# Performance work log

Measured on AMD Instinct MI355X. Metric: run time of the kernel, lower is better.

## Reference

```python
import jax, jax.numpy as jnp
import numpy as np

N, E, D, H, C, K = 100000, 1250000, 64, 64, 40, 2


def setup_inputs() -> dict:
    key = jax.random.key(0)
    ks = jax.random.split(key, 10)
    s_in = 1.0 / np.sqrt(D)
    s_cat = 1.0 / np.sqrt(H * (K + 1))
    return {
        "x": jax.random.normal(ks[0], (N, D), jnp.float32),
        "edge_index": jax.random.randint(ks[1], (2, E), 0, N, dtype=jnp.int64),
        "W_ego": jax.random.normal(ks[2], (D, H), jnp.float32) * s_in,
        "b_ego": jnp.zeros((H,), jnp.float32),
        "W_conv": jax.random.normal(ks[3], (K, D, H), jnp.float32) * s_in,
        "b_conv": jnp.zeros((K, H), jnp.float32),
        "W_cls": jax.random.normal(ks[4], (H * (K + 1), C), jnp.float32) * s_cat,
        "b_cls": jnp.zeros((C,), jnp.float32),
    }


def _gcn_norm(edge_index, n):
    # PyG GCNConv default: add self-loops, symmetric normalization.
    row = jnp.concatenate([edge_index[0], jnp.arange(n, dtype=edge_index.dtype)])
    col = jnp.concatenate([edge_index[1], jnp.arange(n, dtype=edge_index.dtype)])
    deg = jax.ops.segment_sum(jnp.ones_like(col, dtype=jnp.float32), col, num_segments=n)
    dis = jnp.where(deg > 0, jax.lax.rsqrt(jnp.maximum(deg, 1.0)), 0.0)
    norm = dis[row] * dis[col]  # [E+N]
    return row, col, norm


def _gcn_conv(h, W, b, row, col, norm, n):
    hw = h @ W                                   # [N, H] transform first (cheap d)
    msg = norm[:, None] * hw[row]                # gather + scale, [E+N, H]
    agg = jax.ops.segment_sum(msg, col, num_segments=n)  # scatter-add to targets
    return agg + b


def reference(x, edge_index, W_ego, b_ego, W_conv, b_conv, W_cls, b_cls):
    n = x.shape[0]
    row, col, norm = _gcn_norm(edge_index, n)
    parts = [jax.nn.relu(x @ W_ego + b_ego)]
    h = x
    for k in range(K):
        h = jax.nn.relu(_gcn_conv(h, W_conv[k], b_conv[k], row, col, norm, n))
        parts.append(h)
    out = jnp.concatenate(parts, axis=-1)        # [N, H*(K+1)]
    # dropout is identity at inference (training=False)
    return out @ W_cls + b_cls
```

## Files before the change

### kernel.cpp

```cpp
#include <hip/hip_runtime.h>

using u16 = unsigned short;
using u32 = unsigned int;
using u64 = unsigned long long;
using short8 = __attribute__((ext_vector_type(8))) short;
using f32x4  = __attribute__((ext_vector_type(4))) float;

static inline int cdiv(long long a, long long b) { return (int)((a + b - 1) / b); }

__device__ __forceinline__ u16 f2bf(float x) {
    u32 u = __builtin_bit_cast(u32, x);
    u += 0x7fffu + ((u >> 16) & 1u);
    return (u16)(u >> 16);
}
__device__ __forceinline__ float bf2f(u16 h) {
    u32 u = ((u32)h) << 16;
    return __builtin_bit_cast(float, u);
}

#define BKT_SH 10
#define CHUNK 4096

__global__ __launch_bounds__(256) void k_bhist(const int* __restrict__ ei,
                                               int* __restrict__ bcntg, int E) {
    __shared__ int lb[128];
    if (threadIdx.x < 128) lb[threadIdx.x] = 0;
    __syncthreads();
    const int eb = blockIdx.x * CHUNK;
#pragma unroll
    for (int k = 0; k < 16; ++k) {
        int e = eb + k * 256 + threadIdx.x;
        if (e < E) atomicAdd(&lb[ei[E + e] >> BKT_SH], 1);
    }
    __syncthreads();
    if (threadIdx.x < 128 && lb[threadIdx.x] > 0)
        atomicAdd(&bcntg[threadIdx.x], lb[threadIdx.x]);
}

__global__ __launch_bounds__(128) void k_bscan(const int* __restrict__ bcntg,
                                               int* __restrict__ bbase,
                                               int* __restrict__ bcursor, int NB) {
    __shared__ int s[128];
    int t = threadIdx.x;
    int v = (t < NB) ? bcntg[t] : 0;
    s[t] = v;
    __syncthreads();
    for (int st = 1; st < 128; st <<= 1) {
        int add = (t >= st) ? s[t - st] : 0;
        __syncthreads();
        s[t] += add;
        __syncthreads();
    }
    int excl = s[t] - v;
    if (t < NB) { bbase[t] = excl; bcursor[t] = excl; }
    if (t == NB - 1) bbase[NB] = excl + v;
}

__global__ __launch_bounds__(256) void k_passA(const int* __restrict__ ei,
                                               int* __restrict__ bcursor,
                                               u64* __restrict__ sta, int E) {
    __shared__ int lcnt[128];
    __shared__ int lcur[128];
    if (threadIdx.x < 128) lcnt[threadIdx.x] = 0;
    __syncthreads();
    const int eb = blockIdx.x * CHUNK;
    int er[16], ec[16];
#pragma unroll
    for (int k = 0; k < 16; ++k) {
        int e = eb + k * 256 + threadIdx.x;
        if (e < E) {
            er[k] = ei[e];
            ec[k] = ei[E + e];
            atomicAdd(&lcnt[ec[k] >> BKT_SH], 1);
        } else {
            ec[k] = -1;
        }
    }
    __syncthreads();
    if (threadIdx.x < 128)
        lcur[threadIdx.x] = lcnt[threadIdx.x] > 0
                          ? atomicAdd(&bcursor[threadIdx.x], lcnt[threadIdx.x]) : 0;
    __syncthreads();
#pragma unroll
    for (int k = 0; k < 16; ++k) {
        if (ec[k] >= 0) {
            int pos = atomicAdd(&lcur[ec[k] >> BKT_SH], 1);
            sta[pos] = ((u64)(u32)ec[k] << 32) | (u32)er[k];
        }
    }
}

__global__ __launch_bounds__(256) void k_passB(const u64* __restrict__ sta,
                                               const int* __restrict__ bbase,
                                               int* __restrict__ indptr,
                                               float* __restrict__ dis,
                                               int* __restrict__ rows,
                                               int N, int NB) {
    __shared__ int lcnt[1024];
    __shared__ int cur[1024];
    __shared__ int ps[256];
    const int b = blockIdx.x;
    const int t = threadIdx.x;
    const int base = b << BKT_SH;
    const int e0 = bbase[b], e1 = bbase[b + 1];

#pragma unroll
    for (int k = 0; k < 4; ++k) lcnt[k * 256 + t] = 0;
    __syncthreads();
    for (int e = e0 + t; e < e1; e += 256)
        atomicAdd(&lcnt[(int)(sta[e] >> 32) - base], 1);
    __syncthreads();

    int a0 = lcnt[t * 4 + 0], a1 = lcnt[t * 4 + 1];
    int a2 = lcnt[t * 4 + 2], a3 = lcnt[t * 4 + 3];
    int sum = a0 + a1 + a2 + a3;
    ps[t] = sum;
    __syncthreads();
    for (int st = 1; st < 256; st <<= 1) {
        int add = (t >= st) ? ps[t - st] : 0;
        __syncthreads();
        ps[t] += add;
        __syncthreads();
    }
    int ex = e0 + ps[t] - sum;
    int exs[4] = {ex, ex + a0, ex + a0 + a1, ex + a0 + a1 + a2};
    int cnts[4] = {a0, a1, a2, a3};
#pragma unroll
    for (int k = 0; k < 4; ++k) {
        int j = t * 4 + k;
        cur[j] = exs[k];
        int node = base + j;
        if (node < N) {
            indptr[node] = exs[k];
            dis[node] = rsqrtf((float)cnts[k] + 1.0f);
        }
    }
    if (b == NB - 1 && t == 0) indptr[N] = bbase[NB];
    __syncthreads();

    for (int e = e0 + t; e < e1; e += 256) {
        u64 v = sta[e];
        int c = (int)(v >> 32);
        int pos = atomicAdd(&cur[c - base], 1);
        rows[pos] = (int)(u32)v;
    }
}

__global__ __launch_bounds__(256) void k_cast(const float* __restrict__ x,
                                              u32* __restrict__ xb, long long n8) {
    long long t = (long long)blockIdx.x * 256 + threadIdx.x;
    if (t >= n8) return;
    const float4* xp = (const float4*)(x + t * 8);
    float4 v0 = xp[0], v1 = xp[1];
    u32* o = xb + t * 4;
    o[0] = (u32)f2bf(v0.x) | ((u32)f2bf(v0.y) << 16);
    o[1] = (u32)f2bf(v0.z) | ((u32)f2bf(v0.w) << 16);
    o[2] = (u32)f2bf(v1.x) | ((u32)f2bf(v1.y) << 16);
    o[3] = (u32)f2bf(v1.z) | ((u32)f2bf(v1.w) << 16);
}

__global__ __launch_bounds__(256) void k_prep(const float* __restrict__ Wego,
                                              const float* __restrict__ Wconv,
                                              const float* __restrict__ Wcls,
                                              u16* __restrict__ WTin,
                                              u16* __restrict__ WTc0,
                                              u16* __restrict__ WT1,
                                              u16* __restrict__ WT2) {
    int t = blockIdx.x * 256 + threadIdx.x;
    int seg = t >> 6;
    int d = t & 63;
    if (seg < 128) {
        float v = (seg < 64) ? Wconv[d * 64 + seg] : Wego[d * 64 + (seg - 64)];
        WTin[seg * 64 + d] = f2bf(v);
    } else if (seg < 176) {
        int c = seg - 128;
        WTc0[c * 64 + d] = f2bf(c < 40 ? Wcls[d * 40 + c] : 0.f);
    } else if (seg < 288) {
        int c = seg - 176;
        float v = 0.f;
        if (c < 64) v = Wconv[64 * 64 + d * 64 + c];
        else if (c < 104) v = Wcls[(64 + d) * 40 + (c - 64)];
        WT1[c * 64 + d] = f2bf(v);
    } else if (seg < 336) {
        int c = seg - 288;
        WT2[c * 64 + d] = f2bf(c < 40 ? Wcls[(128 + d) * 40 + c] : 0.f);
    }
}

__global__ __launch_bounds__(256) void k_in(const u16* __restrict__ xb,
                                            const u16* __restrict__ WTin,
                                            const float* __restrict__ dis,
                                            const float* __restrict__ bego,
                                            u16* __restrict__ hws1,
                                            u16* __restrict__ p0, int N) {
    const int wid = (blockIdx.x * 256 + threadIdx.x) >> 6;
    const int l = threadIdx.x & 63;
    if (wid * 16 >= N) return;
    const int lr = l & 15;
    const int lk = l >> 4;

    const u16* arow = xb + ((size_t)(wid * 16 + lr)) * 64 + lk * 8;
    short8 a0 = *(const short8*)arow;
    short8 a1 = *(const short8*)(arow + 32);

    float dvals[4];
#pragma unroll
    for (int rg = 0; rg < 4; ++rg) dvals[rg] = dis[wid * 16 + lk * 4 + rg];

    for (int ct = 0; ct < 8; ++ct) {
        const u16* wrow = WTin + ((size_t)(ct * 16 + lr)) * 64 + lk * 8;
        short8 b0 = *(const short8*)wrow;
        short8 b1 = *(const short8*)(wrow + 32);
        f32x4 acc = {0.f, 0.f, 0.f, 0.f};
        acc = __builtin_amdgcn_mfma_f32_16x16x32_bf16(a0, b0, acc, 0, 0, 0);
        acc = __builtin_amdgcn_mfma_f32_16x16x32_bf16(a1, b1, acc, 0, 0, 0);
        const int col = ct * 16 + lr;
        if (col < 64) {
#pragma unroll
            for (int rg = 0; rg < 4; ++rg) {
                int r = wid * 16 + lk * 4 + rg;
                hws1[(size_t)r * 64 + col] = f2bf(dvals[rg] * acc[rg]);
            }
        } else {
            float be = bego[col - 64];
#pragma unroll
            for (int rg = 0; rg < 4; ++rg) {
                int r = wid * 16 + lk * 4 + rg;
                p0[(size_t)r * 64 + (col - 64)] = f2bf(fmaxf(acc[rg] + be, 0.f));
            }
        }
    }
}

__global__ __launch_bounds__(256) void k_cls0(const u16* __restrict__ p0,
                                              const u16* __restrict__ WTc0,
                                              const float* __restrict__ bcls,
                                              float* __restrict__ out, int N) {
    const int wid = (blockIdx.x * 256 + threadIdx.x) >> 6;
    const int l = threadIdx.x & 63;
    if (wid * 16 >= N) return;
    const int lr = l & 15;
    const int lk = l >> 4;

    const u16* arow = p0 + ((size_t)(wid * 16 + lr)) * 64 + lk * 8;
    short8 a0 = *(const short8*)arow;
    short8 a1 = *(const short8*)(arow + 32);

    for (int ct = 0; ct < 3; ++ct) {
        const u16* wrow = WTc0 + ((size_t)(ct * 16 + lr)) * 64 + lk * 8;
        short8 b0 = *(const short8*)wrow;
        short8 b1 = *(const short8*)(wrow + 32);
        f32x4 acc = {0.f, 0.f, 0.f, 0.f};
        acc = __builtin_amdgcn_mfma_f32_16x16x32_bf16(a0, b0, acc, 0, 0, 0);
        acc = __builtin_amdgcn_mfma_f32_16x16x32_bf16(a1, b1, acc, 0, 0, 0);
        const int col = ct * 16 + lr;
        if (col < 40) {
            float bc = bcls[col];
#pragma unroll
            for (int rg = 0; rg < 4; ++rg) {
                int r = wid * 16 + lk * 4 + rg;
                out[(size_t)r * 40 + col] = bc + acc[rg];
            }
        }
    }
}

__global__ __launch_bounds__(512) void k_gather(const int* __restrict__ indptr,
                                                const int* __restrict__ rows,
                                                const float* __restrict__ dis,
                                                const float* __restrict__ bconv,
                                                const u16* __restrict__ hws_in,
                                                u16* __restrict__ h, int N) {
    const int w = threadIdx.x >> 6;
    const int f = threadIdx.x & 63;
    const int i = blockIdx.x * 8 + w;
    if (i >= N) return;

    float acc = bf2f(hws_in[(size_t)i * 64 + f]);
    int p0 = __builtin_amdgcn_readfirstlane(indptr[i]);
    int p1 = __builtin_amdgcn_readfirstlane(indptr[i + 1]);
    int p = p0;
    for (; p + 8 <= p1; p += 8) {
        int r0 = rows[p + 0], r1 = rows[p + 1], r2 = rows[p + 2], r3 = rows[p + 3];
        int r4 = rows[p + 4], r5 = rows[p + 5], r6 = rows[p + 6], r7 = rows[p + 7];
        u16 v0 = hws_in[(size_t)r0 * 64 + f];
        u16 v1 = hws_in[(size_t)r1 * 64 + f];
        u16 v2 = hws_in[(size_t)r2 * 64 + f];
        u16 v3 = hws_in[(size_t)r3 * 64 + f];
        u16 v4 = hws_in[(size_t)r4 * 64 + f];
        u16 v5 = hws_in[(size_t)r5 * 64 + f];
        u16 v6 = hws_in[(size_t)r6 * 64 + f];
        u16 v7 = hws_in[(size_t)r7 * 64 + f];
        acc += ((bf2f(v0) + bf2f(v1)) + (bf2f(v2) + bf2f(v3))) +
               ((bf2f(v4) + bf2f(v5)) + (bf2f(v6) + bf2f(v7)));
    }
    for (; p + 4 <= p1; p += 4) {
        int r0 = rows[p + 0], r1 = rows[p + 1], r2 = rows[p + 2], r3 = rows[p + 3];
        u16 v0 = hws_in[(size_t)r0 * 64 + f];
        u16 v1 = hws_in[(size_t)r1 * 64 + f];
        u16 v2 = hws_in[(size_t)r2 * 64 + f];
        u16 v3 = hws_in[(size_t)r3 * 64 + f];
        acc += (bf2f(v0) + bf2f(v1)) + (bf2f(v2) + bf2f(v3));
    }
    for (; p < p1; ++p) acc += bf2f(hws_in[(size_t)rows[p] * 64 + f]);

    float hv = fmaxf(fmaf(dis[i], acc, bconv[f]), 0.0f);
    h[(size_t)i * 64 + f] = f2bf(hv);
}

template <int NC, bool HAS_NEXT>
__global__ __launch_bounds__(256) void k_mlp(const u16* __restrict__ h,
                                             const u16* __restrict__ WT,
                                             const float* __restrict__ dis,
                                             u16* __restrict__ hws_out,
                                             float* __restrict__ out, int N) {
    const int wid = (blockIdx.x * 256 + threadIdx.x) >> 6;
    const int l = threadIdx.x & 63;
    if (wid * 16 >= N) return;
    const int lr = l & 15;
    const int lk = l >> 4;

    const u16* hrow = h + ((size_t)(wid * 16 + lr)) * 64 + lk * 8;
    short8 a0 = *(const short8*)hrow;
    short8 a1 = *(const short8*)(hrow + 32);

    float dvals[4];
    if (HAS_NEXT) {
#pragma unroll
        for (int rg = 0; rg < 4; ++rg) dvals[rg] = dis[wid * 16 + lk * 4 + rg];
    }

    for (int ct = 0; ct < NC; ++ct) {
        const u16* wrow = WT + ((size_t)(ct * 16 + lr)) * 64 + lk * 8;
        short8 b0 = *(const short8*)wrow;
        short8 b1 = *(const short8*)(wrow + 32);
        f32x4 acc = {0.f, 0.f, 0.f, 0.f};
        acc = __builtin_amdgcn_mfma_f32_16x16x32_bf16(a0, b0, acc, 0, 0, 0);
        acc = __builtin_amdgcn_mfma_f32_16x16x32_bf16(a1, b1, acc, 0, 0, 0);
        const int col = ct * 16 + lr;
#pragma unroll
        for (int rg = 0; rg < 4; ++rg) {
            const int r = wid * 16 + lk * 4 + rg;
            if (HAS_NEXT) {
                if (col < 64) {
                    hws_out[(size_t)r * 64 + col] = f2bf(dvals[rg] * acc[rg]);
                } else {
                    int oc = col - 64;
                    if (oc < 40) out[(size_t)r * 40 + oc] += acc[rg];
                }
            } else {
                if (col < 40) out[(size_t)r * 40 + col] += acc[rg];
            }
        }
    }
}

extern "C" void kernel_launch(void* const* d_in, const int* in_sizes, int n_in,
                              void* d_out, int out_size, void* d_ws, size_t ws_size,
                              hipStream_t stream) {
    const float* x     = (const float*)d_in[0];
    const int*   ei    = (const int*)d_in[1];
    const float* Wego  = (const float*)d_in[2];
    const float* bego  = (const float*)d_in[3];
    const float* Wconv = (const float*)d_in[4];
    const float* bconv = (const float*)d_in[5];
    const float* Wcls  = (const float*)d_in[6];
    const float* bcls  = (const float*)d_in[7];
    float* out = (float*)d_out;

    const int N = in_sizes[0] / 64;
    const int E = in_sizes[1] / 2;
    const int NB = cdiv(N, 1 << BKT_SH);

    u16* xb   = (u16*)d_ws;
    u64* sta  = (u64*)d_ws;
    u16* hws1 = xb + (size_t)N * 64;
    u16* hws2 = hws1 + (size_t)N * 64;
    u16* hp   = hws2 + (size_t)N * 64;
    u16* WTin = hp + (size_t)N * 64;
    u16* WTc0 = WTin + 128 * 64;
    u16* WT1  = WTc0 + 48 * 64;
    u16* WT2  = WT1 + 112 * 64;
    float* dis = (float*)(WT2 + 48 * 64);
    int* indptr  = (int*)(dis + N);
    int* bcntg   = indptr + N + 1024;
    int* bbase   = bcntg + 128;
    int* bcursor = bbase + 132;
    int* rows    = bcursor + 128;

    hipMemsetAsync(bcntg, 0, 128 * sizeof(int), stream);

    k_bhist<<<cdiv(E, CHUNK), 256, 0, stream>>>(ei, bcntg, E);
    k_bscan<<<1, 128, 0, stream>>>(bcntg, bbase, bcursor, NB);
    k_passA<<<cdiv(E, CHUNK), 256, 0, stream>>>(ei, bcursor, sta, E);
    k_passB<<<NB, 256, 0, stream>>>(sta, bbase, indptr, dis, rows, N, NB);

    k_cast<<<cdiv((long long)N * 8, 256), 256, 0, stream>>>(x, (u32*)xb, (long long)N * 8);
    k_prep<<<cdiv(336 * 64, 256), 256, 0, stream>>>(Wego, Wconv, Wcls, WTin, WTc0, WT1, WT2);
    k_in<<<cdiv(cdiv(N, 16), 4), 256, 0, stream>>>(xb, WTin, dis, bego, hws1, hp, N);
    k_cls0<<<cdiv(cdiv(N, 16), 4), 256, 0, stream>>>(hp, WTc0, bcls, out, N);

    const int n_rt = cdiv(N, 16);
    k_gather<<<cdiv(N, 8), 512, 0, stream>>>(indptr, rows, dis, bconv, hws1, hp, N);
    k_mlp<7, true><<<cdiv(n_rt, 4), 256, 0, stream>>>(hp, WT1, dis, hws2, out, N);
    k_gather<<<cdiv(N, 8), 512, 0, stream>>>(indptr, rows, dis, bconv + 64, hws2, hp, N);
    k_mlp<3, false><<<cdiv(n_rt, 4), 256, 0, stream>>>(hp, WT2, dis, nullptr, out, N);
}
```

Baseline: 223.3 us.

## Fuse classifier into one concatenated GEMM, pack sort keys to 32 bits, drop cast kernel

The sort keys shrink from 64-bit (col,row) pairs to 32-bit words holding the local column in the high bits and the row in the low 17 bits. This halves the sort-buffer traffic but assumes N < 2^17. The bf16 cast of x is folded into the input GEMM kernel, and the three partial classifier GEMMs, which did read-modify-write on the fp32 output, are replaced by one final GEMM over a concatenated [N,192] hidden buffer. The aim is fewer launches and less output traffic, at the cost of a wider strided hidden buffer.

```diff
diff --git a/kernel.cpp b/kernel.cpp
--- a/kernel.cpp
+++ b/kernel.cpp
@@ -2,7 +2,6 @@
 
 using u16 = unsigned short;
 using u32 = unsigned int;
-using u64 = unsigned long long;
 using short8 = __attribute__((ext_vector_type(8))) short;
 using f32x4  = __attribute__((ext_vector_type(4))) float;
 
@@ -19,6 +18,7 @@
 }
 
 #define BKT_SH 10
+#define BKT_MASK ((1 << BKT_SH) - 1)
 #define CHUNK 4096
 
 __global__ __launch_bounds__(256) void k_bhist(const int* __restrict__ ei,
@@ -58,7 +58,7 @@
 
 __global__ __launch_bounds__(256) void k_passA(const int* __restrict__ ei,
                                                int* __restrict__ bcursor,
-                                               u64* __restrict__ sta, int E) {
+                                               u32* __restrict__ sta, int E) {
     __shared__ int lcnt[128];
     __shared__ int lcur[128];
     if (threadIdx.x < 128) lcnt[threadIdx.x] = 0;
@@ -85,12 +85,12 @@
     for (int k = 0; k < 16; ++k) {
         if (ec[k] >= 0) {
             int pos = atomicAdd(&lcur[ec[k] >> BKT_SH], 1);
-            sta[pos] = ((u64)(u32)ec[k] << 32) | (u32)er[k];
-        }
-    }
-}
-
-__global__ __launch_bounds__(256) void k_passB(const u64* __restrict__ sta,
+            sta[pos] = ((u32)(ec[k] & BKT_MASK) << 17) | (u32)er[k];
+        }
+    }
+}
+
+__global__ __launch_bounds__(256) void k_passB(const u32* __restrict__ sta,
                                                const int* __restrict__ bbase,
                                                int* __restrict__ indptr,
                                                float* __restrict__ dis,
@@ -108,7 +108,7 @@
     for (int k = 0; k < 4; ++k) lcnt[k * 256 + t] = 0;
     __syncthreads();
     for (int e = e0 + t; e < e1; e += 256)
-        atomicAdd(&lcnt[(int)(sta[e] >> 32) - base], 1);
+        atomicAdd(&lcnt[sta[e] >> 17], 1);
     __syncthreads();
 
     int a0 = lcnt[t * 4 + 0], a1 = lcnt[t * 4 + 1];
@@ -139,73 +139,69 @@
     __syncthreads();
 
     for (int e = e0 + t; e < e1; e += 256) {
-        u64 v = sta[e];
-        int c = (int)(v >> 32);
-        int pos = atomicAdd(&cur[c - base], 1);
-        rows[pos] = (int)(u32)v;
-    }
-}
-
-__global__ __launch_bounds__(256) void k_cast(const float* __restrict__ x,
-                                              u32* __restrict__ xb, long long n8) {
-    long long t = (long long)blockIdx.x * 256 + threadIdx.x;
-    if (t >= n8) return;
-    const float4* xp = (const float4*)(x + t * 8);
-    float4 v0 = xp[0], v1 = xp[1];
-    u32* o = xb + t * 4;
-    o[0] = (u32)f2bf(v0.x) | ((u32)f2bf(v0.y) << 16);
-    o[1] = (u32)f2bf(v0.z) | ((u32)f2bf(v0.w) << 16);
-    o[2] = (u32)f2bf(v1.x) | ((u32)f2bf(v1.y) << 16);
-    o[3] = (u32)f2bf(v1.z) | ((u32)f2bf(v1.w) << 16);
+        u32 v = sta[e];
+        int pos = atomicAdd(&cur[v >> 17], 1);
+        rows[pos] = (int)(v & 0x1FFFF);
+    }
 }
 
 __global__ __launch_bounds__(256) void k_prep(const float* __restrict__ Wego,
                                               const float* __restrict__ Wconv,
                                               const float* __restrict__ Wcls,
                                               u16* __restrict__ WTin,
-                                              u16* __restrict__ WTc0,
                                               u16* __restrict__ WT1,
-                                              u16* __restrict__ WT2) {
+                                              u16* __restrict__ WcatT) {
     int t = blockIdx.x * 256 + threadIdx.x;
-    int seg = t >> 6;
-    int d = t & 63;
-    if (seg < 128) {
+    if (t < 128 * 64) {
+        int seg = t >> 6, d = t & 63;
         float v = (seg < 64) ? Wconv[d * 64 + seg] : Wego[d * 64 + (seg - 64)];
-        WTin[seg * 64 + d] = f2bf(v);
-    } else if (seg < 176) {
-        int c = seg - 128;
-        WTc0[c * 64 + d] = f2bf(c < 40 ? Wcls[d * 40 + c] : 0.f);
-    } else if (seg < 288) {
-        int c = seg - 176;
-        float v = 0.f;
-        if (c < 64) v = Wconv[64 * 64 + d * 64 + c];
-        else if (c < 104) v = Wcls[(64 + d) * 40 + (c - 64)];
-        WT1[c * 64 + d] = f2bf(v);
-    } else if (seg < 336) {
-        int c = seg - 288;
-        WT2[c * 64 + d] = f2bf(c < 40 ? Wcls[(128 + d) * 40 + c] : 0.f);
-    }
-}
-
-__global__ __launch_bounds__(256) void k_in(const u16* __restrict__ xb,
+        WTin[t] = f2bf(v);
+    } else if (t < 128 * 64 + 64 * 64) {
+        int u = t - 128 * 64;
+        int c = u >> 6, d = u & 63;
+        WT1[u] = f2bf(Wconv[64 * 64 + d * 64 + c]);
+    } else if (t < 128 * 64 + 64 * 64 + 48 * 192) {
+        int u = t - (128 * 64 + 64 * 64);
+        int c = u / 192, d = u - c * 192;
+        WcatT[u] = f2bf(c < 40 ? Wcls[d * 40 + c] : 0.f);
+    }
+}
+
+__global__ __launch_bounds__(256) void k_in(const float* __restrict__ x,
                                             const u16* __restrict__ WTin,
                                             const float* __restrict__ dis,
                                             const float* __restrict__ bego,
-                                            u16* __restrict__ hws1,
-                                            u16* __restrict__ p0, int N) {
+                                            u16* __restrict__ hws,
+                                            u16* __restrict__ hall, int N) {
     const int wid = (blockIdx.x * 256 + threadIdx.x) >> 6;
     const int l = threadIdx.x & 63;
     if (wid * 16 >= N) return;
     const int lr = l & 15;
     const int lk = l >> 4;
 
-    const u16* arow = xb + ((size_t)(wid * 16 + lr)) * 64 + lk * 8;
-    short8 a0 = *(const short8*)arow;
-    short8 a1 = *(const short8*)(arow + 32);
+    int r_ld = wid * 16 + lr;
+    if (r_ld >= N) r_ld = N - 1;
+    const float* xrow = x + (size_t)r_ld * 64 + lk * 8;
+    float4 u0 = *(const float4*)(xrow);
+    float4 u1 = *(const float4*)(xrow + 4);
+    float4 u2 = *(const float4*)(xrow + 32);
+    float4 u3 = *(const float4*)(xrow + 36);
+    short8 a0, a1;
+    a0[0] = (short)f2bf(u0.x); a0[1] = (short)f2bf(u0.y);
+    a0[2] = (short)f2bf(u0.z); a0[3] = (short)f2bf(u0.w);
+    a0[4] = (short)f2bf(u1.x); a0[5] = (short)f2bf(u1.y);
+    a0[6] = (short)f2bf(u1.z); a0[7] = (short)f2bf(u1.w);
+    a1[0] = (short)f2bf(u2.x); a1[1] = (short)f2bf(u2.y);
+    a1[2] = (short)f2bf(u2.z); a1[3] = (short)f2bf(u2.w);
+    a1[4] = (short)f2bf(u3.x); a1[5] = (short)f2bf(u3.y);
+    a1[6] = (short)f2bf(u3.z); a1[7] = (short)f2bf(u3.w);
 
     float dvals[4];
 #pragma unroll
-    for (int rg = 0; rg < 4; ++rg) dvals[rg] = dis[wid * 16 + lk * 4 + rg];
+    for (int rg = 0; rg < 4; ++rg) {
+        int r = wid * 16 + lk * 4 + rg;
+        dvals[rg] = dis[r < N ? r : N - 1];
+    }
 
     for (int ct = 0; ct < 8; ++ct) {
         const u16* wrow = WTin + ((size_t)(ct * 16 + lr)) * 64 + lk * 8;
@@ -219,47 +215,14 @@
 #pragma unroll
             for (int rg = 0; rg < 4; ++rg) {
                 int r = wid * 16 + lk * 4 + rg;
-                hws1[(size_t)r * 64 + col] = f2bf(dvals[rg] * acc[rg]);
+                if (r < N) hws[(size_t)r * 64 + col] = f2bf(dvals[rg] * acc[rg]);
             }
         } else {
             float be = bego[col - 64];
 #pragma unroll
             for (int rg = 0; rg < 4; ++rg) {
                 int r = wid * 16 + lk * 4 + rg;
-                p0[(size_t)r * 64 + (col - 64)] = f2bf(fmaxf(acc[rg] + be, 0.f));
-            }
-        }
-    }
-}
-
-__global__ __launch_bounds__(256) void k_cls0(const u16* __restrict__ p0,
-                                              const u16* __restrict__ WTc0,
-                                              const float* __restrict__ bcls,
-                                              float* __restrict__ out, int N) {
-    const int wid = (blockIdx.x * 256 + threadIdx.x) >> 6;
-    const int l = threadIdx.x & 63;
-    if (wid * 16 >= N) return;
-    const int lr = l & 15;
-    const int lk = l >> 4;
-
-    const u16* arow = p0 + ((size_t)(wid * 16 + lr)) * 64 + lk * 8;
-    short8 a0 = *(const short8*)arow;
-    short8 a1 = *(const short8*)(arow + 32);
-
-    for (int ct = 0; ct < 3; ++ct) {
-        const u16* wrow = WTc0 + ((size_t)(ct * 16 + lr)) * 64 + lk * 8;
-        short8 b0 = *(const short8*)wrow;
-        short8 b1 = *(const short8*)(wrow + 32);
-        f32x4 acc = {0.f, 0.f, 0.f, 0.f};
-        acc = __builtin_amdgcn_mfma_f32_16x16x32_bf16(a0, b0, acc, 0, 0, 0);
-        acc = __builtin_amdgcn_mfma_f32_16x16x32_bf16(a1, b1, acc, 0, 0, 0);
-        const int col = ct * 16 + lr;
-        if (col < 40) {
-            float bc = bcls[col];
-#pragma unroll
-            for (int rg = 0; rg < 4; ++rg) {
-                int r = wid * 16 + lk * 4 + rg;
-                out[(size_t)r * 40 + col] = bc + acc[rg];
+                if (r < N) hall[(size_t)r * 192 + (col - 64)] = f2bf(fmaxf(acc[rg] + be, 0.f));
             }
         }
     }
@@ -270,7 +233,7 @@
                                                 const float* __restrict__ dis,
                                                 const float* __restrict__ bconv,
                                                 const u16* __restrict__ hws_in,
-                                                u16* __restrict__ h, int N) {
+                                                u16* __restrict__ hdst, int N) {
     const int w = threadIdx.x >> 6;
     const int f = threadIdx.x & 63;
     const int i = blockIdx.x * 8 + w;
@@ -305,33 +268,34 @@
     for (; p < p1; ++p) acc += bf2f(hws_in[(size_t)rows[p] * 64 + f]);
 
     float hv = fmaxf(fmaf(dis[i], acc, bconv[f]), 0.0f);
-    h[(size_t)i * 64 + f] = f2bf(hv);
-}
-
-template <int NC, bool HAS_NEXT>
-__global__ __launch_bounds__(256) void k_mlp(const u16* __restrict__ h,
-                                             const u16* __restrict__ WT,
-                                             const float* __restrict__ dis,
-                                             u16* __restrict__ hws_out,
-                                             float* __restrict__ out, int N) {
+    hdst[(size_t)i * 192 + f] = f2bf(hv);
+}
+
+__global__ __launch_bounds__(256) void k_next1(const u16* __restrict__ hall,
+                                               const u16* __restrict__ WT1,
+                                               const float* __restrict__ dis,
+                                               u16* __restrict__ hws, int N) {
     const int wid = (blockIdx.x * 256 + threadIdx.x) >> 6;
     const int l = threadIdx.x & 63;
     if (wid * 16 >= N) return;
     const int lr = l & 15;
     const int lk = l >> 4;
 
-    const u16* hrow = h + ((size_t)(wid * 16 + lr)) * 64 + lk * 8;
-    short8 a0 = *(const short8*)hrow;
-    short8 a1 = *(const short8*)(hrow + 32);
+    int r_ld = wid * 16 + lr;
+    if (r_ld >= N) r_ld = N - 1;
+    const u16* arow = hall + (size_t)r_ld * 192 + 64 + lk * 8;
+    short8 a0 = *(const short8*)arow;
+    short8 a1 = *(const short8*)(arow + 32);
 
     float dvals[4];
-    if (HAS_NEXT) {
-#pragma unroll
-        for (int rg = 0; rg < 4; ++rg) dvals[rg] = dis[wid * 16 + lk * 4 + rg];
-    }
-
-    for (int ct = 0; ct < NC; ++ct) {
-        const u16* wrow = WT + ((size_t)(ct * 16 + lr)) * 64 + lk * 8;
+#pragma unroll
+    for (int rg = 0; rg < 4; ++rg) {
+        int r = wid * 16 + lk * 4 + rg;
+        dvals[rg] = dis[r < N ? r : N - 1];
+    }
+
+    for (int ct = 0; ct < 4; ++ct) {
+        const u16* wrow = WT1 + ((size_t)(ct * 16 + lr)) * 64 + lk * 8;
         short8 b0 = *(const short8*)wrow;
         short8 b1 = *(const short8*)(wrow + 32);
         f32x4 acc = {0.f, 0.f, 0.f, 0.f};
@@ -340,16 +304,44 @@
         const int col = ct * 16 + lr;
 #pragma unroll
         for (int rg = 0; rg < 4; ++rg) {
-            const int r = wid * 16 + lk * 4 + rg;
-            if (HAS_NEXT) {
-                if (col < 64) {
-                    hws_out[(size_t)r * 64 + col] = f2bf(dvals[rg] * acc[rg]);
-                } else {
-                    int oc = col - 64;
-                    if (oc < 40) out[(size_t)r * 40 + oc] += acc[rg];
-                }
-            } else {
-                if (col < 40) out[(size_t)r * 40 + col] += acc[rg];
+            int r = wid * 16 + lk * 4 + rg;
+            if (r < N) hws[(size_t)r * 64 + col] = f2bf(dvals[rg] * acc[rg]);
+        }
+    }
+}
+
+__global__ __launch_bounds__(256) void k_clsall(const u16* __restrict__ hall,
+                                                const u16* __restrict__ WcatT,
+                                                const float* __restrict__ bcls,
+                                                float* __restrict__ out, int N) {
+    const int wid = (blockIdx.x * 256 + threadIdx.x) >> 6;
+    const int l = threadIdx.x & 63;
+    if (wid * 16 >= N) return;
+    const int lr = l & 15;
+    const int lk = l >> 4;
+
+    int r_ld = wid * 16 + lr;
+    if (r_ld >= N) r_ld = N - 1;
+    const u16* arow = hall + (size_t)r_ld * 192 + lk * 8;
+    short8 a[6];
+#pragma unroll
+    for (int kt = 0; kt < 6; ++kt) a[kt] = *(const short8*)(arow + kt * 32);
+
+    for (int ct = 0; ct < 3; ++ct) {
+        const u16* brow = WcatT + ((size_t)(ct * 16 + lr)) * 192 + lk * 8;
+        f32x4 acc = {0.f, 0.f, 0.f, 0.f};
+#pragma unroll
+        for (int kt = 0; kt < 6; ++kt) {
+            short8 b = *(const short8*)(brow + kt * 32);
+            acc = __builtin_amdgcn_mfma_f32_16x16x32_bf16(a[kt], b, acc, 0, 0, 0);
+        }
+        const int col = ct * 16 + lr;
+        if (col < 40) {
+            float bc = bcls[col];
+#pragma unroll
+            for (int rg = 0; rg < 4; ++rg) {
+                int r = wid * 16 + lk * 4 + rg;
+                if (r < N) out[(size_t)r * 40 + col] = bc + acc[rg];
             }
         }
     }
@@ -372,18 +364,15 @@
     const int E = in_sizes[1] / 2;
     const int NB = cdiv(N, 1 << BKT_SH);
 
-    u16* xb   = (u16*)d_ws;
-    u64* sta  = (u64*)d_ws;
-    u16* hws1 = xb + (size_t)N * 64;
-    u16* hws2 = hws1 + (size_t)N * 64;
-    u16* hp   = hws2 + (size_t)N * 64;
-    u16* WTin = hp + (size_t)N * 64;
-    u16* WTc0 = WTin + 128 * 64;
-    u16* WT1  = WTc0 + 48 * 64;
-    u16* WT2  = WT1 + 112 * 64;
-    float* dis = (float*)(WT2 + 48 * 64);
+    u16* hall   = (u16*)d_ws;
+    u32* sta    = (u32*)d_ws;
+    u16* hwsbuf = hall + (size_t)N * 192;
+    u16* WTin   = hwsbuf + (size_t)N * 64;
+    u16* WT1    = WTin + 128 * 64;
+    u16* WcatT  = WT1 + 64 * 64;
+    float* dis  = (float*)(WcatT + 48 * 192);
     int* indptr  = (int*)(dis + N);
-    int* bcntg   = indptr + N + 1024;
+    int* bcntg   = indptr + N + 64;
     int* bbase   = bcntg + 128;
     int* bcursor = bbase + 132;
     int* rows    = bcursor + 128;
@@ -395,14 +384,17 @@
     k_passA<<<cdiv(E, CHUNK), 256, 0, stream>>>(ei, bcursor, sta, E);
     k_passB<<<NB, 256, 0, stream>>>(sta, bbase, indptr, dis, rows, N, NB);
 
-    k_cast<<<cdiv((long long)N * 8, 256), 256, 0, stream>>>(x, (u32*)xb, (long long)N * 8);
-    k_prep<<<cdiv(336 * 64, 256), 256, 0, stream>>>(Wego, Wconv, Wcls, WTin, WTc0, WT1, WT2);
-    k_in<<<cdiv(cdiv(N, 16), 4), 256, 0, stream>>>(xb, WTin, dis, bego, hws1, hp, N);
-    k_cls0<<<cdiv(cdiv(N, 16), 4), 256, 0, stream>>>(hp, WTc0, bcls, out, N);
-
-    const int n_rt = cdiv(N, 16);
-    k_gather<<<cdiv(N, 8), 512, 0, stream>>>(indptr, rows, dis, bconv, hws1, hp, N);
-    k_mlp<7, true><<<cdiv(n_rt, 4), 256, 0, stream>>>(hp, WT1, dis, hws2, out, N);
-    k_gather<<<cdiv(N, 8), 512, 0, stream>>>(indptr, rows, dis, bconv + 64, hws2, hp, N);
-    k_mlp<3, false><<<cdiv(n_rt, 4), 256, 0, stream>>>(hp, WT2, dis, nullptr, out, N);
-}
+    k_prep<<<cdiv(128 * 64 + 64 * 64 + 48 * 192, 256), 256, 0, stream>>>(
+        Wego, Wconv, Wcls, WTin, WT1, WcatT);
+    const int n_blk16 = cdiv(cdiv(N, 16), 4);
+    k_in<<<n_blk16, 256, 0, stream>>>(x, WTin, dis, bego, hwsbuf, hall, N);
+
+    k_gather<<<cdiv(N, 8), 512, 0, stream>>>(indptr, rows, dis, bconv,
+                                             hwsbuf, hall + 64, N);
+    k_next1<<<n_blk16, 256, 0, stream>>>(hall, WT1, dis, hwsbuf, N);
+
+    k_gather<<<cdiv(N, 8), 512, 0, stream>>>(indptr, rows, dis, bconv + 64,
+                                             hwsbuf, hall + 128, N);
+
+    k_clsall<<<n_blk16, 256, 0, stream>>>(hall, WcatT, bcls, out, N);
+}
```

After: 215.3 us. 3.6% less time.
